# Kernel optimization log

Measured on AMD Instinct MI355X. Metric: run time of the kernel, lower is better.

Reference implementation:

```python
import jax, jax.numpy as jnp
import numpy as np

V = 32000   # vocab_size
L = 4       # n_layer
H = 12      # n_head
C = 768     # n_embd
T = 1024    # block_size / seq len
B = 4       # batch
D = C // H  # head_dim
F = 4 * C   # mlp hidden


def setup_inputs() -> dict:
    key = jax.random.key(0)
    ks = jax.random.split(key, 12)
    n = lambda k, sh: (jax.random.normal(k, sh, dtype=jnp.float32) * 0.02)
    return {
        "idx": jax.random.randint(ks[0], (B, T), 0, V, dtype=jnp.int32),
        "tok_emb": n(ks[1], (V, C)),
        "pos_emb": n(ks[2], (T, C)),
        "Wq": n(ks[3], (L, C, C)),
        "Wk": n(ks[4], (L, C, C)),
        "Wv": n(ks[5], (L, C, C)),
        "Wp": n(ks[6], (L, C, C)),
        "bp": jnp.zeros((L, C), jnp.float32),
        "ln1s": jnp.ones((L, C), jnp.float32),
        "ln1b": jnp.zeros((L, C), jnp.float32),
        "ln2s": jnp.ones((L, C), jnp.float32),
        "ln2b": jnp.zeros((L, C), jnp.float32),
        "W1": n(ks[7], (L, C, F)),
        "b1": jnp.zeros((L, F), jnp.float32),
        "W2": n(ks[8], (L, F, C)),
        "b2": jnp.zeros((L, C), jnp.float32),
        "lnfs": jnp.ones((C,), jnp.float32),
        "lnfb": jnp.zeros((C,), jnp.float32),
        "Whead": n(ks[9], (C, V)),
    }


def _ln(x, s, b):
    m = x.mean(-1, keepdims=True)
    v = ((x - m) ** 2).mean(-1, keepdims=True)
    return (x - m) * jax.lax.rsqrt(v + 1e-5) * s + b


def reference(idx, tok_emb, pos_emb, Wq, Wk, Wv, Wp, bp, ln1s, ln1b, ln2s, ln2b,
              W1, b1, W2, b2, lnfs, lnfb, Whead):
    Bc, Tc = idx.shape
    x = tok_emb[idx] + pos_emb[None, :Tc]               # [B,T,C]
    mask = jnp.tril(jnp.ones((Tc, Tc), bool))           # causal mask
    scale = 1.0 / np.sqrt(D)
    for l in range(L):
        # --- causal self-attention (explicit QK^T, masked softmax) ---
        h = _ln(x, ln1s[l], ln1b[l])
        q = (h @ Wq[l]).reshape(Bc, Tc, H, D).transpose(0, 2, 1, 3)  # [B,H,T,D]
        k = (h @ Wk[l]).reshape(Bc, Tc, H, D).transpose(0, 2, 1, 3)
        v = (h @ Wv[l]).reshape(Bc, Tc, H, D).transpose(0, 2, 1, 3)
        att = jnp.einsum('bhqd,bhkd->bhqk', q, k) * scale            # [B,H,T,T]
        att = jnp.where(mask, att, -jnp.inf)
        att = jax.nn.softmax(att, axis=-1)
        y = jnp.einsum('bhqk,bhkd->bhqd', att, v)
        y = y.transpose(0, 2, 1, 3).reshape(Bc, Tc, C)
        x = x + (y @ Wp[l] + bp[l])
        # --- GELU MLP ---
        h = _ln(x, ln2s[l], ln2b[l])
        x = x + (jax.nn.gelu(h @ W1[l] + b1[l], approximate=False) @ W2[l] + b2[l])
    x = _ln(x, lnfs, lnfb)
    logits = x @ Whead                                  # [B,T,V]
    return logits
```

## Files before the change

### kernel.cpp

```cpp
#include <hip/hip_runtime.h>
#include <stdint.h>

#define B_ 4
#define T_ 1024
#define C_ 768
#define H_ 12
#define D_ 64
#define F_ 3072
#define V_ 32000
#define L_ 4

typedef unsigned short ushort_t;
typedef __bf16 bf16x8 __attribute__((ext_vector_type(8)));
typedef float f32x4 __attribute__((ext_vector_type(4)));
typedef unsigned short u16x8 __attribute__((ext_vector_type(8)));

__device__ __forceinline__ float b2f(unsigned short u) {
    union { unsigned int i; float f; } x; x.i = ((unsigned int)u) << 16; return x.f;
}
__device__ __forceinline__ unsigned short f2b(float f) {
    union { float f; unsigned int i; } x; x.f = f;
    unsigned int r = x.i + 0x7FFFu + ((x.i >> 16) & 1u);
    return (unsigned short)(r >> 16);
}

__device__ __forceinline__ float gelu_f(float u) {
    float z = fabsf(u) * 0.70710678118654752f;
    float t = __builtin_amdgcn_rcpf(1.0f + 0.3275911f * z);
    float poly = t * (0.254829592f + t * (-0.284496736f + t * (1.421413741f +
                 t * (-1.453152027f + t * 1.061405429f))));
    float erfz = 1.0f - poly * __expf(-z * z);
    return u * 0.5f * (1.0f + copysignf(erfz, u));
}

__device__ __forceinline__ void gload16(const ushort_t* g, ushort_t* l) {
    __builtin_amdgcn_global_load_lds(
        (const __attribute__((address_space(1))) unsigned int*)g,
        (__attribute__((address_space(3))) unsigned int*)l, 16, 0, 0);
}

__global__ __launch_bounds__(256) void k_embed(const int* __restrict__ idx,
        const float* __restrict__ tok, const float* __restrict__ pos,
        ushort_t* __restrict__ x) {
    int i = blockIdx.x * 256 + threadIdx.x;
    int m = i / (C_ / 4);
    int cc = (i % (C_ / 4)) * 4;
    int t = m & (T_ - 1);
    int tokid = idx[m];
    float4 te = *(const float4*)&tok[(size_t)tokid * C_ + cc];
    float4 pe = *(const float4*)&pos[(size_t)t * C_ + cc];
    ushort4 o;
    o.x = f2b(te.x + pe.x); o.y = f2b(te.y + pe.y);
    o.z = f2b(te.z + pe.z); o.w = f2b(te.w + pe.w);
    *(ushort4*)&x[(size_t)m * C_ + cc] = o;
}

__global__ __launch_bounds__(256) void k_ln(const ushort_t* __restrict__ x,
        const float* __restrict__ s, const float* __restrict__ b,
        ushort_t* __restrict__ out) {
    const int lane = threadIdx.x & 63, wave = threadIdx.x >> 6;
    const int row = blockIdx.x * 4 + wave;
    const ushort_t* xr = x + (size_t)row * C_;
    float vf[3][4];
    float sum = 0.f, sq = 0.f;
#pragma unroll
    for (int j = 0; j < 3; ++j) {
        ushort4 u = *(const ushort4*)&xr[lane * 4 + j * 256];
        vf[j][0] = b2f(u.x); vf[j][1] = b2f(u.y); vf[j][2] = b2f(u.z); vf[j][3] = b2f(u.w);
#pragma unroll
        for (int e = 0; e < 4; ++e) { sum += vf[j][e]; sq += vf[j][e] * vf[j][e]; }
    }
#pragma unroll
    for (int off = 1; off < 64; off <<= 1) {
        sum += __shfl_xor(sum, off);
        sq  += __shfl_xor(sq,  off);
    }
    float mean = sum * (1.f / C_);
    float var  = sq * (1.f / C_) - mean * mean;
    float rstd = rsqrtf(var + 1e-5f);
#pragma unroll
    for (int j = 0; j < 3; ++j) {
        int c = lane * 4 + j * 256;
        float4 sv = *(const float4*)&s[c];
        float4 bv = *(const float4*)&b[c];
        ushort4 o;
        o.x = f2b((vf[j][0] - mean) * rstd * sv.x + bv.x);
        o.y = f2b((vf[j][1] - mean) * rstd * sv.y + bv.y);
        o.z = f2b((vf[j][2] - mean) * rstd * sv.z + bv.z);
        o.w = f2b((vf[j][3] - mean) * rstd * sv.w + bv.w);
        *(ushort4*)&out[(size_t)row * C_ + c] = o;
    }
}

__global__ void k_tcvt(const float* __restrict__ in, ushort_t* __restrict__ out,
                       int R, int C) {
    __shared__ float tile[32][33];
    const float* src = in + (size_t)blockIdx.z * R * C;
    ushort_t* dst = out + (size_t)blockIdx.z * R * C;
    int r0 = blockIdx.y * 32, c0 = blockIdx.x * 32;
    int tx = threadIdx.x, ty = threadIdx.y;
#pragma unroll
    for (int i = ty; i < 32; i += 8)
        tile[i][tx] = src[(size_t)(r0 + i) * C + c0 + tx];
    __syncthreads();
#pragma unroll
    for (int i = ty; i < 32; i += 8)
        dst[(size_t)(c0 + i) * R + r0 + tx] = f2b(tile[tx][i]);
}

__global__ void k_tcvt16(const float* __restrict__ wq, const float* __restrict__ wk,
                         const float* __restrict__ wv, const float* __restrict__ wp,
                         ushort_t* __restrict__ out) {
    __shared__ float tile[32][33];
    int l = blockIdx.z >> 2, w = blockIdx.z & 3;
    const float* src = (w == 0 ? wq : w == 1 ? wk : w == 2 ? wv : wp) + (size_t)l * C_ * C_;
    ushort_t* dst = out + (size_t)blockIdx.z * C_ * C_;
    int r0 = blockIdx.y * 32, c0 = blockIdx.x * 32;
    int tx = threadIdx.x, ty = threadIdx.y;
#pragma unroll
    for (int i = ty; i < 32; i += 8)
        tile[i][tx] = src[(size_t)(r0 + i) * C_ + c0 + tx];
    __syncthreads();
#pragma unroll
    for (int i = ty; i < 32; i += 8)
        dst[(size_t)(c0 + i) * C_ + r0 + tx] = f2b(tile[tx][i]);
}

template <int EPI>
__global__ __launch_bounds__(256) void k_gemm(
        const ushort_t* __restrict__ A, const ushort_t* __restrict__ BT,
        const float* __restrict__ bias, const float* __restrict__ resid,
        float* __restrict__ outf, ushort_t* __restrict__ outb,
        ushort_t* __restrict__ outb2, ushort_t* __restrict__ outb3,
        int M, int N, int K) {
    __shared__ __align__(16) ushort_t S[24576];
    const int tid = threadIdx.x;
    const int lane = tid & 63, wave = tid >> 6;
    const int lr = lane & 15, lg = lane >> 4;
    const int wm = (wave >> 1) * 64, wn = (wave & 1) * 64;

    const int bid = blockIdx.x;
    const int m_in = bid & 7;
    const int strip = (bid >> 3) & 3;
    const int ncol = bid >> 5;
    const int m0 = (strip * 8 + m_in) << 7;
    const int n0 = ncol << 7;

    const int sr = wave * 16 + (lane >> 2);
    const int sc = (((lane & 3) ^ ((lane >> 3) & 3)) << 3);

    f32x4 acc[4][4];
#pragma unroll
    for (int i = 0; i < 4; ++i)
#pragma unroll
        for (int j = 0; j < 4; ++j) acc[i][j] = (f32x4){0.f, 0.f, 0.f, 0.f};

    auto stage = [&](int k0, int buf) {
        ushort_t* as = S + buf * 4096;
        ushort_t* bs = S + 12288 + buf * 4096;
        gload16(&A [(size_t)(m0 + sr)      * K + k0 + sc], as + (wave * 16) * 32);
        gload16(&A [(size_t)(m0 + 64 + sr) * K + k0 + sc], as + (64 + wave * 16) * 32);
        gload16(&BT[(size_t)(n0 + sr)      * K + k0 + sc], bs + (wave * 16) * 32);
        gload16(&BT[(size_t)(n0 + 64 + sr) * K + k0 + sc], bs + (64 + wave * 16) * 32);
    };

    const int nt = K >> 5;
    stage(0, 0);
    stage(32, 1);
    int cur = 0, pre = 2;
    const int swzr = (lr >> 1) & 3;
    for (int t = 0; t < nt; ++t) {
        if (t + 1 < nt) asm volatile("s_waitcnt vmcnt(4)" ::: "memory");
        else            asm volatile("s_waitcnt vmcnt(0)" ::: "memory");
        __builtin_amdgcn_sched_barrier(0);
        __builtin_amdgcn_s_barrier();
        const ushort_t* as = S + cur * 4096;
        const ushort_t* bs = S + 12288 + cur * 4096;
        bf16x8 af[4], bfr[4];
#pragma unroll
        for (int i = 0; i < 4; ++i)
            af[i]  = *(const bf16x8*)&as[(wm + i * 16 + lr) * 32 + ((lg ^ swzr) << 3)];
#pragma unroll
        for (int j = 0; j < 4; ++j)
            bfr[j] = *(const bf16x8*)&bs[(wn + j * 16 + lr) * 32 + ((lg ^ swzr) << 3)];
        if (t + 2 < nt) stage((t + 2) << 5, pre);
#pragma unroll
        for (int i = 0; i < 4; ++i)
#pragma unroll
            for (int j = 0; j < 4; ++j)
                acc[i][j] = __builtin_amdgcn_mfma_f32_16x16x32_bf16(af[i], bfr[j], acc[i][j], 0, 0, 0);
        cur = (cur == 2) ? 0 : cur + 1;
        pre = (pre == 2) ? 0 : pre + 1;
    }

    if (EPI == 2) {
        float* cls = (float*)S;
#pragma unroll
        for (int h = 0; h < 2; ++h) {
            __syncthreads();
            if ((wm >> 6) == h) {
#pragma unroll
                for (int i = 0; i < 4; ++i)
#pragma unroll
                    for (int j = 0; j < 4; ++j)
#pragma unroll
                        for (int r = 0; r < 4; ++r)
                            cls[(i * 16 + lg * 4 + r) * 128 + wn + j * 16 + lr] = acc[i][j][r];
            }
            __syncthreads();
#pragma unroll
            for (int p = 0; p < 4; ++p) {
                int idx = p * 256 + tid;
                int row = idx >> 4;
                int colc = (idx & 15) * 8;
                f32x4 v0 = *(const f32x4*)&cls[row * 128 + colc];
                f32x4 v1 = *(const f32x4*)&cls[row * 128 + colc + 4];
                size_t gidx = (size_t)(m0 + h * 64 + row) * N + n0 + colc;
                u16x8 rv = *(const u16x8*)&outb2[gidx];
                f32x4 b0 = *(const f32x4*)&bias[n0 + colc];
                f32x4 b1 = *(const f32x4*)&bias[n0 + colc + 4];
                u16x8 o;
#pragma unroll
                for (int e = 0; e < 4; ++e) o[e]     = f2b(v0[e] + b0[e] + b2f(rv[e]));
#pragma unroll
                for (int e = 0; e < 4; ++e) o[4 + e] = f2b(v1[e] + b1[e] + b2f(rv[4 + e]));
                *(u16x8*)&outb[gidx] = o;
            }
        }
        return;
    }

    if (EPI == 1) {
        ushort_t* cls = S;
        __syncthreads();
#pragma unroll
        for (int i = 0; i < 4; ++i)
#pragma unroll
            for (int j = 0; j < 4; ++j) {
                float bval = bias[n0 + wn + j * 16 + lr];
#pragma unroll
                for (int r = 0; r < 4; ++r)
                    cls[(wm + i * 16 + lg * 4 + r) * 128 + wn + j * 16 + lr] =
                        f2b(gelu_f(acc[i][j][r] + bval));
            }
        __syncthreads();
#pragma unroll
        for (int p = 0; p < 8; ++p) {
            int row = p * 16 + (tid >> 4);
            int colc = (tid & 15) * 8;
            u16x8 val = *(const u16x8*)&cls[row * 128 + colc];
            *(u16x8*)&outb[(size_t)(m0 + row) * N + n0 + colc] = val;
        }
        return;
    }

    if (EPI == 3) {
        const int region = n0 / 768;
        const int c0 = n0 % 768;
        const int bb = m0 >> 10, t0 = m0 & 1023;
        ushort_t* cls = S;
        if (region < 2) {
            ushort_t* dst = (region == 0) ? outb : outb2;
            __syncthreads();
#pragma unroll
            for (int i = 0; i < 4; ++i)
#pragma unroll
                for (int j = 0; j < 4; ++j)
#pragma unroll
                    for (int r = 0; r < 4; ++r)
                        cls[(wm + i * 16 + lg * 4 + r) * 136 + wn + j * 16 + lr] =
                            f2b(acc[i][j][r]);
            __syncthreads();
#pragma unroll
            for (int p = 0; p < 8; ++p) {
                int row = p * 16 + (tid >> 4);
                int colc = (tid & 15) * 8;
                u16x8 val = *(const u16x8*)&cls[row * 136 + colc];
                int hh = (c0 + colc) >> 6, d = (c0 + colc) & 63;
                *(u16x8*)&dst[((((size_t)bb * H_ + hh) << 10) + t0 + row) * D_ + d] = val;
            }
        } else {
            __syncthreads();
#pragma unroll
            for (int i = 0; i < 4; ++i)
#pragma unroll
                for (int j = 0; j < 4; ++j)
#pragma unroll
                    for (int r = 0; r < 4; ++r)
                        cls[(wn + j * 16 + lr) * 136 + wm + i * 16 + lg * 4 + r] =
                            f2b(acc[i][j][r]);
            __syncthreads();
#pragma unroll
            for (int p = 0; p < 8; ++p) {
                int col = p * 16 + (tid >> 4);
                int rowc = (tid & 15) * 8;
                u16x8 val = *(const u16x8*)&cls[col * 136 + rowc];
                int hh = (c0 + col) >> 6, d = (c0 + col) & 63;
                *(u16x8*)&outb3[(((size_t)bb * H_ + hh) * D_ + d) * T_ + t0 + rowc] = val;
            }
        }
        return;
    }
}

__global__ __launch_bounds__(512, 4) void k_gemmh(
        const ushort_t* __restrict__ A, const ushort_t* __restrict__ BT,
        float* __restrict__ outf, int M, int N, int K) {
    __shared__ __align__(16) ushort_t S[36864];
    const int tid = threadIdx.x;
    const int lane = tid & 63, wave = tid >> 6;
    const int lr = lane & 15, lg = lane >> 4;
    const int wm = (wave >> 2) * 64, wn = (wave & 3) * 64;

    const int bid = blockIdx.x;
    const int m_in = bid & 7;
    const int strip = (bid >> 3) & 3;
    const int ncol = bid >> 5;
    const int m0 = (strip * 8 + m_in) << 7;
    const int n0 = ncol << 8;

    const int srr = lane >> 2;
    const int sc = (((lane & 3) ^ ((lane >> 3) & 3)) << 3);

    f32x4 acc[4][4];
#pragma unroll
    for (int i = 0; i < 4; ++i)
#pragma unroll
        for (int j = 0; j < 4; ++j) acc[i][j] = (f32x4){0.f, 0.f, 0.f, 0.f};

    auto stage = [&](int k0, int buf) {
        ushort_t* as = S + buf * 4096;
        ushort_t* bs = S + 12288 + buf * 8192;
        gload16(&A [(size_t)(m0 + wave * 16 + srr) * K + k0 + sc], as + (wave * 16) * 32);
        gload16(&BT[(size_t)(n0 + wave * 32 + srr)      * K + k0 + sc], bs + (wave * 32) * 32);
        gload16(&BT[(size_t)(n0 + wave * 32 + 16 + srr) * K + k0 + sc], bs + (wave * 32 + 16) * 32);
    };

    const int nt = K >> 5;
    stage(0, 0);
    stage(32, 1);
    int cur = 0, pre = 2;
    const int swzr = (lr >> 1) & 3;
    for (int t = 0; t < nt; ++t) {
        if (t + 1 < nt) asm volatile("s_waitcnt vmcnt(3)" ::: "memory");
        else            asm volatile("s_waitcnt vmcnt(0)" ::: "memory");
        __builtin_amdgcn_sched_barrier(0);
        __builtin_amdgcn_s_barrier();
        const ushort_t* as = S + cur * 4096;
        const ushort_t* bs = S + 12288 + cur * 8192;
        bf16x8 af[4], bfr[4];
#pragma unroll
        for (int i = 0; i < 4; ++i)
            af[i]  = *(const bf16x8*)&as[(wm + i * 16 + lr) * 32 + ((lg ^ swzr) << 3)];
#pragma unroll
        for (int j = 0; j < 4; ++j)
            bfr[j] = *(const bf16x8*)&bs[(wn + j * 16 + lr) * 32 + ((lg ^ swzr) << 3)];
        if (t + 2 < nt) stage((t + 2) << 5, pre);
#pragma unroll
        for (int i = 0; i < 4; ++i)
#pragma unroll
            for (int j = 0; j < 4; ++j)
                acc[i][j] = __builtin_amdgcn_mfma_f32_16x16x32_bf16(af[i], bfr[j], acc[i][j], 0, 0, 0);
        cur = (cur == 2) ? 0 : cur + 1;
        pre = (pre == 2) ? 0 : pre + 1;
    }

    float* cls = (float*)S;
#pragma unroll
    for (int h = 0; h < 2; ++h) {
        __syncthreads();
        if ((wm >> 6) == h) {
#pragma unroll
            for (int i = 0; i < 4; ++i)
#pragma unroll
                for (int j = 0; j < 4; ++j)
#pragma unroll
                    for (int r = 0; r < 4; ++r)
                        cls[(i * 16 + lg * 4 + r) * 260 + wn + j * 16 + lr] = acc[i][j][r];
        }
        __syncthreads();
#pragma unroll
        for (int p = 0; p < 8; ++p) {
            int idx = p * 512 + tid;
            int row = idx >> 6;
            int colc = (idx & 63) * 4;
            f32x4 val = *(const f32x4*)&cls[row * 260 + colc];
            __builtin_nontemporal_store(val,
                (f32x4*)&outf[(size_t)(m0 + h * 64 + row) * N + n0 + colc]);
        }
    }
}

__global__ __launch_bounds__(256) void k_attn(const ushort_t* __restrict__ q,
        const ushort_t* __restrict__ k, const ushort_t* __restrict__ vT,
        ushort_t* __restrict__ yc) {
    __shared__ __align__(16) ushort_t P[4][16 * 136];
    const int lane = threadIdx.x & 63, wave = threadIdx.x >> 6;
    const int lr = lane & 15, lg = lane >> 4;
    const int bh = blockIdx.x;
    const int bb = bh / H_, hh = bh % H_;
    const int qrow0 = (gridDim.y - 1 - blockIdx.y) * 64 + wave * 16;
    const ushort_t* qb = q + (size_t)bh * T_ * D_;
    const ushort_t* kb = k + (size_t)bh * T_ * D_;
    const ushort_t* vb = vT + (size_t)bh * D_ * T_;

    bf16x8 aq0 = *(const bf16x8*)&qb[(qrow0 + lr) * D_ + lg * 8];
    bf16x8 aq1 = *(const bf16x8*)&qb[(qrow0 + lr) * D_ + 32 + lg * 8];

    f32x4 accY[4];
    float ls = 0.f;
#pragma unroll
    for (int d = 0; d < 4; ++d) accY[d] = (f32x4){0.f, 0.f, 0.f, 0.f};

    ushort_t* pw = &P[wave][0];
    const int kv_end = qrow0 + 16;
    for (int kv0 = 0; kv0 < kv_end; kv0 += 128) {
        const bool full = (kv0 + 127 <= qrow0);
        float p[8][4];
        float ps = 0.f;
#pragma unroll
        for (int j = 0; j < 8; ++j) {
            f32x4 s = (f32x4){0.f, 0.f, 0.f, 0.f};
            bf16x8 bk0 = *(const bf16x8*)&kb[(kv0 + j * 16 + lr) * D_ + lg * 8];
            bf16x8 bk1 = *(const bf16x8*)&kb[(kv0 + j * 16 + lr) * D_ + 32 + lg * 8];
            __builtin_amdgcn_s_setprio(1);
            s = __builtin_amdgcn_mfma_f32_16x16x32_bf16(bk0, aq0, s, 0, 0, 0);
            s = __builtin_amdgcn_mfma_f32_16x16x32_bf16(bk1, aq1, s, 0, 0, 0);
            __builtin_amdgcn_s_setprio(0);
            if (full) {
#pragma unroll
                for (int r = 0; r < 4; ++r) { p[j][r] = __expf(s[r] * 0.125f); ps += p[j][r]; }
            } else {
                int kcb = kv0 + j * 16 + lg * 4;
#pragma unroll
                for (int r = 0; r < 4; ++r) {
                    p[j][r] = (kcb + r <= qrow0 + lr) ? __expf(s[r] * 0.125f) : 0.f;
                    ps += p[j][r];
                }
            }
        }
        ps += __shfl_xor(ps, 16);
        ps += __shfl_xor(ps, 32);
        ls += ps;

        asm volatile("s_waitcnt lgkmcnt(0)" ::: "memory");
        __builtin_amdgcn_sched_barrier(0);
#pragma unroll
        for (int j = 0; j < 8; ++j) {
            unsigned int w0, w1;
            asm("v_cvt_pk_bf16_f32 %0, %1, %2" : "=v"(w0) : "v"(p[j][0]), "v"(p[j][1]));
            asm("v_cvt_pk_bf16_f32 %0, %1, %2" : "=v"(w1) : "v"(p[j][2]), "v"(p[j][3]));
            uint2 w; w.x = w0; w.y = w1;
            *(uint2*)&pw[lr * 136 + j * 16 + lg * 4] = w;
        }
        asm volatile("s_waitcnt lgkmcnt(0)" ::: "memory");
        __builtin_amdgcn_sched_barrier(0);
        bf16x8 pa[4];
#pragma unroll
        for (int ks = 0; ks < 4; ++ks)
            pa[ks] = *(const bf16x8*)&pw[lr * 136 + ks * 32 + lg * 8];
#pragma unroll
        for (int d = 0; d < 4; ++d) {
            __builtin_amdgcn_s_setprio(1);
#pragma unroll
            for (int ks = 0; ks < 4; ++ks) {
                bf16x8 bv = *(const bf16x8*)&vb[(d * 16 + lr) * T_ + kv0 + ks * 32 + lg * 8];
                accY[d] = __builtin_amdgcn_mfma_f32_16x16x32_bf16(pa[ks], bv, accY[d], 0, 0, 0);
            }
            __builtin_amdgcn_s_setprio(0);
        }
    }
    float inv[4];
#pragma unroll
    for (int r = 0; r < 4; ++r) inv[r] = 1.0f / __shfl(ls, lg * 4 + r);

    asm volatile("s_waitcnt lgkmcnt(0)" ::: "memory");
    __builtin_amdgcn_sched_barrier(0);
#pragma unroll
    for (int d = 0; d < 4; ++d)
#pragma unroll
        for (int r = 0; r < 4; ++r)
            pw[(lg * 4 + r) * 72 + d * 16 + lr] = f2b(accY[d][r] * inv[r]);
    asm volatile("s_waitcnt lgkmcnt(0)" ::: "memory");
    __builtin_amdgcn_sched_barrier(0);
#pragma unroll
    for (int p = 0; p < 2; ++p) {
        int row = p * 8 + (lane >> 3);
        int colc = (lane & 7) * 8;
        u16x8 val = *(const u16x8*)&pw[row * 72 + colc];
        *(u16x8*)&yc[((size_t)bb * T_ + qrow0 + row) * C_ + hh * D_ + colc] = val;
    }
}

extern "C" void kernel_launch(void* const* d_in, const int* in_sizes, int n_in,
                              void* d_out, int out_size, void* d_ws, size_t ws_size,
                              hipStream_t stream) {
    (void)in_sizes; (void)n_in; (void)out_size; (void)ws_size;
    const int*   idx  = (const int*)d_in[0];
    const float* tok  = (const float*)d_in[1];
    const float* pos  = (const float*)d_in[2];
    const float* Wq   = (const float*)d_in[3];
    const float* Wk   = (const float*)d_in[4];
    const float* Wv   = (const float*)d_in[5];
    const float* Wp   = (const float*)d_in[6];
    const float* bp   = (const float*)d_in[7];
    const float* ln1s = (const float*)d_in[8];
    const float* ln1b = (const float*)d_in[9];
    const float* ln2s = (const float*)d_in[10];
    const float* ln2b = (const float*)d_in[11];
    const float* W1   = (const float*)d_in[12];
    const float* b1   = (const float*)d_in[13];
    const float* W2   = (const float*)d_in[14];
    const float* b2   = (const float*)d_in[15];
    const float* lnfs = (const float*)d_in[16];
    const float* lnfb = (const float*)d_in[17];
    const float* Wh   = (const float*)d_in[18];
    float* out = (float*)d_out;

    char* ws = (char*)d_ws;
    size_t off = 0;
    auto alloc = [&](size_t bytes) { void* p = ws + off; off += (bytes + 255) & ~(size_t)255; return p; };

    const size_t CCE = (size_t)C_ * C_;
    const size_t CFE = (size_t)C_ * F_;
    ushort_t* wCC  = (ushort_t*)alloc(16 * CCE * 2);
    ushort_t* w1T  = (ushort_t*)alloc((size_t)L_ * CFE * 2);
    ushort_t* w2T  = (ushort_t*)alloc((size_t)L_ * CFE * 2);
    ushort_t* whT  = (ushort_t*)alloc((size_t)C_ * V_ * 2);
    ushort_t* x    = (ushort_t*)alloc((size_t)B_ * T_ * C_ * 2);
    ushort_t* h    = (ushort_t*)alloc((size_t)B_ * T_ * C_ * 2);
    ushort_t* qb_  = (ushort_t*)alloc((size_t)B_ * T_ * C_ * 2);
    ushort_t* kb_  = (ushort_t*)alloc((size_t)B_ * T_ * C_ * 2);
    ushort_t* vTb  = (ushort_t*)alloc((size_t)B_ * T_ * C_ * 2);
    ushort_t* yc   = (ushort_t*)alloc((size_t)B_ * T_ * C_ * 2);
    ushort_t* mh   = (ushort_t*)alloc((size_t)B_ * T_ * F_ * 2);

    dim3 tb(32, 8);
    k_tcvt16<<<dim3(24, 24, 16), tb, 0, stream>>>(Wq, Wk, Wv, Wp, wCC);
    k_tcvt<<<dim3(96, 24, 4), tb, 0, stream>>>(W1, w1T, C_, F_);
    k_tcvt<<<dim3(24, 96, 4), tb, 0, stream>>>(W2, w2T, F_, C_);
    k_tcvt<<<dim3(1000, 24, 1), tb, 0, stream>>>(Wh, whT, C_, V_);

    k_embed<<<3072, 256, 0, stream>>>(idx, tok, pos, x);

    for (int l = 0; l < L_; ++l) {
        k_ln<<<1024, 256, 0, stream>>>(x, ln1s + l * C_, ln1b + l * C_, h);
        k_gemm<3><<<18 * 32, 256, 0, stream>>>(h, wCC + (size_t)(l * 4) * CCE,
            nullptr, nullptr, nullptr, qb_, kb_, vTb, 4096, 3 * C_, C_);
        k_attn<<<dim3(48, 16), 256, 0, stream>>>(qb_, kb_, vTb, yc);
        k_gemm<2><<<6 * 32, 256, 0, stream>>>(yc, wCC + (size_t)(l * 4 + 3) * CCE,
            bp + l * C_, nullptr, nullptr, x, x, nullptr, 4096, C_, C_);
        k_ln<<<1024, 256, 0, stream>>>(x, ln2s + l * C_, ln2b + l * C_, h);
        k_gemm<1><<<24 * 32, 256, 0, stream>>>(h, w1T + (size_t)l * CFE,
            b1 + l * F_, nullptr, nullptr, mh, nullptr, nullptr, 4096, F_, C_);
        k_gemm<2><<<6 * 32, 256, 0, stream>>>(mh, w2T + (size_t)l * CFE,
            b2 + l * C_, nullptr, nullptr, x, x, nullptr, 4096, C_, F_);
    }
    k_ln<<<1024, 256, 0, stream>>>(x, lnfs, lnfb, h);
    k_gemmh<<<4000, 512, 0, stream>>>(h, whT, out, 4096, V_, C_);
}
```

Baseline: 1.036 ms.

## Process two 16-row query tiles per wave in attention to reuse K/V loads

Each attention wave now handles 32 query rows (two 16-row MFMA tiles) instead of 16. Every K and V fragment loaded from global memory feeds two sets of MFMAs, and the grid is halved along the query axis. The P conversion to bf16 is now done inside the score loop and kept in registers until the LDS store. The cost is higher register pressure and LDS use, fewer blocks (384 vs 768), and coarser causal work per wave, which may reduce occupancy and worsen load balance.

```diff
diff --git a/kernel.cpp b/kernel.cpp
--- a/kernel.cpp
+++ b/kernel.cpp
@@ -394,97 +394,132 @@
 __global__ __launch_bounds__(256) void k_attn(const ushort_t* __restrict__ q,
         const ushort_t* __restrict__ k, const ushort_t* __restrict__ vT,
         ushort_t* __restrict__ yc) {
-    __shared__ __align__(16) ushort_t P[4][16 * 136];
+    __shared__ __align__(16) ushort_t P[4][32 * 136];
     const int lane = threadIdx.x & 63, wave = threadIdx.x >> 6;
     const int lr = lane & 15, lg = lane >> 4;
     const int bh = blockIdx.x;
     const int bb = bh / H_, hh = bh % H_;
-    const int qrow0 = (gridDim.y - 1 - blockIdx.y) * 64 + wave * 16;
+    const int qrow0 = (gridDim.y - 1 - blockIdx.y) * 128 + wave * 32;
     const ushort_t* qb = q + (size_t)bh * T_ * D_;
     const ushort_t* kb = k + (size_t)bh * T_ * D_;
     const ushort_t* vb = vT + (size_t)bh * D_ * T_;
 
-    bf16x8 aq0 = *(const bf16x8*)&qb[(qrow0 + lr) * D_ + lg * 8];
-    bf16x8 aq1 = *(const bf16x8*)&qb[(qrow0 + lr) * D_ + 32 + lg * 8];
-
-    f32x4 accY[4];
-    float ls = 0.f;
-#pragma unroll
-    for (int d = 0; d < 4; ++d) accY[d] = (f32x4){0.f, 0.f, 0.f, 0.f};
+    bf16x8 aq0A = *(const bf16x8*)&qb[(qrow0 + lr) * D_ + lg * 8];
+    bf16x8 aq1A = *(const bf16x8*)&qb[(qrow0 + lr) * D_ + 32 + lg * 8];
+    bf16x8 aq0B = *(const bf16x8*)&qb[(qrow0 + 16 + lr) * D_ + lg * 8];
+    bf16x8 aq1B = *(const bf16x8*)&qb[(qrow0 + 16 + lr) * D_ + 32 + lg * 8];
+
+    f32x4 accA[4], accB[4];
+    float lsA = 0.f, lsB = 0.f;
+#pragma unroll
+    for (int d = 0; d < 4; ++d) {
+        accA[d] = (f32x4){0.f, 0.f, 0.f, 0.f};
+        accB[d] = (f32x4){0.f, 0.f, 0.f, 0.f};
+    }
 
     ushort_t* pw = &P[wave][0];
-    const int kv_end = qrow0 + 16;
+    const int kv_end = qrow0 + 32;
     for (int kv0 = 0; kv0 < kv_end; kv0 += 128) {
-        const bool full = (kv0 + 127 <= qrow0);
-        float p[8][4];
-        float ps = 0.f;
+        const bool fullA = (kv0 + 127 <= qrow0);
+        const bool fullB = (kv0 + 127 <= qrow0 + 16);
+        uint2 wA[8], wB[8];
+        float psA = 0.f, psB = 0.f;
 #pragma unroll
         for (int j = 0; j < 8; ++j) {
-            f32x4 s = (f32x4){0.f, 0.f, 0.f, 0.f};
             bf16x8 bk0 = *(const bf16x8*)&kb[(kv0 + j * 16 + lr) * D_ + lg * 8];
             bf16x8 bk1 = *(const bf16x8*)&kb[(kv0 + j * 16 + lr) * D_ + 32 + lg * 8];
+            f32x4 sA = (f32x4){0.f, 0.f, 0.f, 0.f};
+            f32x4 sB = (f32x4){0.f, 0.f, 0.f, 0.f};
             __builtin_amdgcn_s_setprio(1);
-            s = __builtin_amdgcn_mfma_f32_16x16x32_bf16(bk0, aq0, s, 0, 0, 0);
-            s = __builtin_amdgcn_mfma_f32_16x16x32_bf16(bk1, aq1, s, 0, 0, 0);
+            sA = __builtin_amdgcn_mfma_f32_16x16x32_bf16(bk0, aq0A, sA, 0, 0, 0);
+            sA = __builtin_amdgcn_mfma_f32_16x16x32_bf16(bk1, aq1A, sA, 0, 0, 0);
+            sB = __builtin_amdgcn_mfma_f32_16x16x32_bf16(bk0, aq0B, sB, 0, 0, 0);
+            sB = __builtin_amdgcn_mfma_f32_16x16x32_bf16(bk1, aq1B, sB, 0, 0, 0);
             __builtin_amdgcn_s_setprio(0);
-            if (full) {
-#pragma unroll
-                for (int r = 0; r < 4; ++r) { p[j][r] = __expf(s[r] * 0.125f); ps += p[j][r]; }
+            float pA[4], pB[4];
+            const int kcb = kv0 + j * 16 + lg * 4;
+            if (fullA) {
+#pragma unroll
+                for (int r = 0; r < 4; ++r) { pA[r] = __expf(sA[r] * 0.125f); psA += pA[r]; }
             } else {
-                int kcb = kv0 + j * 16 + lg * 4;
 #pragma unroll
                 for (int r = 0; r < 4; ++r) {
-                    p[j][r] = (kcb + r <= qrow0 + lr) ? __expf(s[r] * 0.125f) : 0.f;
-                    ps += p[j][r];
+                    pA[r] = (kcb + r <= qrow0 + lr) ? __expf(sA[r] * 0.125f) : 0.f;
+                    psA += pA[r];
                 }
             }
-        }
-        ps += __shfl_xor(ps, 16);
-        ps += __shfl_xor(ps, 32);
-        ls += ps;
+            if (fullB) {
+#pragma unroll
+                for (int r = 0; r < 4; ++r) { pB[r] = __expf(sB[r] * 0.125f); psB += pB[r]; }
+            } else {
+#pragma unroll
+                for (int r = 0; r < 4; ++r) {
+                    pB[r] = (kcb + r <= qrow0 + 16 + lr) ? __expf(sB[r] * 0.125f) : 0.f;
+                    psB += pB[r];
+                }
+            }
+            unsigned int w0, w1;
+            asm("v_cvt_pk_bf16_f32 %0, %1, %2" : "=v"(w0) : "v"(pA[0]), "v"(pA[1]));
+            asm("v_cvt_pk_bf16_f32 %0, %1, %2" : "=v"(w1) : "v"(pA[2]), "v"(pA[3]));
+            wA[j].x = w0; wA[j].y = w1;
+            asm("v_cvt_pk_bf16_f32 %0, %1, %2" : "=v"(w0) : "v"(pB[0]), "v"(pB[1]));
+            asm("v_cvt_pk_bf16_f32 %0, %1, %2" : "=v"(w1) : "v"(pB[2]), "v"(pB[3]));
+            wB[j].x = w0; wB[j].y = w1;
+        }
+        psA += __shfl_xor(psA, 16);
+        psA += __shfl_xor(psA, 32);
+        lsA += psA;
+        psB += __shfl_xor(psB, 16);
+        psB += __shfl_xor(psB, 32);
+        lsB += psB;
 
         asm volatile("s_waitcnt lgkmcnt(0)" ::: "memory");
         __builtin_amdgcn_sched_barrier(0);
 #pragma unroll
         for (int j = 0; j < 8; ++j) {
-            unsigned int w0, w1;
-            asm("v_cvt_pk_bf16_f32 %0, %1, %2" : "=v"(w0) : "v"(p[j][0]), "v"(p[j][1]));
-            asm("v_cvt_pk_bf16_f32 %0, %1, %2" : "=v"(w1) : "v"(p[j][2]), "v"(p[j][3]));
-            uint2 w; w.x = w0; w.y = w1;
-            *(uint2*)&pw[lr * 136 + j * 16 + lg * 4] = w;
+            *(uint2*)&pw[lr * 136 + j * 16 + lg * 4]        = wA[j];
+            *(uint2*)&pw[(16 + lr) * 136 + j * 16 + lg * 4] = wB[j];
         }
         asm volatile("s_waitcnt lgkmcnt(0)" ::: "memory");
         __builtin_amdgcn_sched_barrier(0);
-        bf16x8 pa[4];
-#pragma unroll
-        for (int ks = 0; ks < 4; ++ks)
-            pa[ks] = *(const bf16x8*)&pw[lr * 136 + ks * 32 + lg * 8];
+        bf16x8 paA[4], paB[4];
+#pragma unroll
+        for (int ks = 0; ks < 4; ++ks) {
+            paA[ks] = *(const bf16x8*)&pw[lr * 136 + ks * 32 + lg * 8];
+            paB[ks] = *(const bf16x8*)&pw[(16 + lr) * 136 + ks * 32 + lg * 8];
+        }
 #pragma unroll
         for (int d = 0; d < 4; ++d) {
             __builtin_amdgcn_s_setprio(1);
 #pragma unroll
             for (int ks = 0; ks < 4; ++ks) {
                 bf16x8 bv = *(const bf16x8*)&vb[(d * 16 + lr) * T_ + kv0 + ks * 32 + lg * 8];
-                accY[d] = __builtin_amdgcn_mfma_f32_16x16x32_bf16(pa[ks], bv, accY[d], 0, 0, 0);
+                accA[d] = __builtin_amdgcn_mfma_f32_16x16x32_bf16(paA[ks], bv, accA[d], 0, 0, 0);
+                accB[d] = __builtin_amdgcn_mfma_f32_16x16x32_bf16(paB[ks], bv, accB[d], 0, 0, 0);
             }
             __builtin_amdgcn_s_setprio(0);
         }
     }
-    float inv[4];
-#pragma unroll
-    for (int r = 0; r < 4; ++r) inv[r] = 1.0f / __shfl(ls, lg * 4 + r);
+    float invA[4], invB[4];
+#pragma unroll
+    for (int r = 0; r < 4; ++r) {
+        invA[r] = 1.0f / __shfl(lsA, lg * 4 + r);
+        invB[r] = 1.0f / __shfl(lsB, lg * 4 + r);
+    }
 
     asm volatile("s_waitcnt lgkmcnt(0)" ::: "memory");
     __builtin_amdgcn_sched_barrier(0);
 #pragma unroll
     for (int d = 0; d < 4; ++d)
 #pragma unroll
-        for (int r = 0; r < 4; ++r)
-            pw[(lg * 4 + r) * 72 + d * 16 + lr] = f2b(accY[d][r] * inv[r]);
+        for (int r = 0; r < 4; ++r) {
+            pw[(lg * 4 + r) * 72 + d * 16 + lr]        = f2b(accA[d][r] * invA[r]);
+            pw[(16 + lg * 4 + r) * 72 + d * 16 + lr]   = f2b(accB[d][r] * invB[r]);
+        }
     asm volatile("s_waitcnt lgkmcnt(0)" ::: "memory");
     __builtin_amdgcn_sched_barrier(0);
 #pragma unroll
-    for (int p = 0; p < 2; ++p) {
+    for (int p = 0; p < 4; ++p) {
         int row = p * 8 + (lane >> 3);
         int colc = (lane & 7) * 8;
         u16x8 val = *(const u16x8*)&pw[row * 72 + colc];
@@ -547,7 +582,7 @@
         k_ln<<<1024, 256, 0, stream>>>(x, ln1s + l * C_, ln1b + l * C_, h);
         k_gemm<3><<<18 * 32, 256, 0, stream>>>(h, wCC + (size_t)(l * 4) * CCE,
             nullptr, nullptr, nullptr, qb_, kb_, vTb, 4096, 3 * C_, C_);
-        k_attn<<<dim3(48, 16), 256, 0, stream>>>(qb_, kb_, vTb, yc);
+        k_attn<<<dim3(48, 8), 256, 0, stream>>>(qb_, kb_, vTb, yc);
         k_gemm<2><<<6 * 32, 256, 0, stream>>>(yc, wCC + (size_t)(l * 4 + 3) * CCE,
             bp + l * C_, nullptr, nullptr, x, x, nullptr, 4096, C_, C_);
         k_ln<<<1024, 256, 0, stream>>>(x, ln2s + l * C_, ln2b + l * C_, h);
```

Result: faster. 1.014 ms, median of 2 (-2.2%).
